# Optimization experiments

Hardware: AMD Instinct MI355X
Metric: run time of the kernel (lower is better)

The kernel has to match this reference:

```python
import jax, jax.numpy as jnp
import numpy as np

T, U, I, B, K = 64, 142, 4500, 16384, 10


def setup_inputs() -> dict:
    key = jax.random.key(0)
    k1, k2, k3, k4, k5, k6 = jax.random.split(key, 6)
    q = jax.random.uniform(k1, (T, U, I), dtype=jnp.float32, minval=0.01, maxval=5.0)
    miss = jax.random.uniform(k2, (T, U, I)) < 0.3
    qos_tensor = jnp.where(miss, 0.0, q)
    # user_avg exactly as in __init__: sum over items / count of rated items (clamped >= 1)
    cnt = jnp.clip((qos_tensor > 0).sum(axis=2).astype(jnp.float32), 1.0, None)
    user_avg = qos_tensor.sum(axis=2) / cnt  # [T, U]
    # time-aggregated similarity: random symmetric matrix in [-1, 1]
    s = jax.random.uniform(k3, (U, U), dtype=jnp.float32, minval=-1.0, maxval=1.0)
    user_sim_agg = 0.5 * (s + s.T)
    user_id = jax.random.randint(k4, (B,), 0, U)
    item_id = jax.random.randint(k5, (B,), 0, I)
    time_id = jax.random.randint(k6, (B,), 0, T)
    return {
        "qos_tensor": qos_tensor,
        "user_avg": user_avg,
        "user_sim_agg": user_sim_agg,
        "user_id": user_id,
        "item_id": item_id,
        "time_id": time_id,
        "top_k": K,
    }


def reference(qos_tensor, user_avg, user_sim_agg, user_id, item_id, time_id, top_k):
    num_users = qos_tensor.shape[1]
    avg_u = user_avg[time_id, user_id]                      # [B]
    sim_u = user_sim_agg[user_id]                           # [B, U]
    # ratings of every user for (time_id, item_id): column gather, [B, U]
    u_idx = jnp.arange(num_users)[None, :]
    item_col = qos_tensor[time_id[:, None], u_idx, item_id[:, None]]
    item_rated = item_col > 0                               # [B, U]
    sim_m = jnp.where(item_rated, sim_u, 0.0)
    top_sim, top_user = jax.lax.top_k(sim_m, top_k)         # [B, K]
    top_sim = top_sim / (top_sim.sum(axis=1, keepdims=True) + 1e-8)
    top_sim = jnp.nan_to_num(top_sim)
    # neighbor ratings and neighbor averages
    r_vs = qos_tensor[time_id[:, None], top_user, item_id[:, None]]  # [B, K]
    avg_v = user_avg[time_id[:, None], top_user]                     # [B, K]
    pred = avg_u + (top_sim * (r_vs - avg_v)).sum(axis=1)            # [B]
    return pred
```

## Files before the change

kernel.cpp:

```cpp
#include <hip/hip_runtime.h>
#include <math.h>

#define T_DIM 64
#define U_DIM 142
#define I_DIM 4500
#define B_DIM 16384
#define K_TOP 10

__global__ __launch_bounds__(256) void ucf_kernel(
    const float* __restrict__ qos,
    const float* __restrict__ user_avg,
    const float* __restrict__ user_sim,
    const int*   __restrict__ user_id,
    const int*   __restrict__ item_id,
    const int*   __restrict__ time_id,
    float*       __restrict__ out)
{
    const int lane = threadIdx.x & 63;
    const int wid  = threadIdx.x >> 6;
    const int b    = blockIdx.x * 4 + wid;
    if (b >= B_DIM) return;

    const int u = user_id[b];
    const int i = item_id[b];
    const int t = time_id[b];

    const float* qcol = qos + ((size_t)t * U_DIM) * (size_t)I_DIM + i;
    const float* srow = user_sim + (size_t)u * U_DIM;
    const float* arow = user_avg + (size_t)t * U_DIM;

    float val[3];
    float con[3];
#pragma unroll
    for (int j = 0; j < 3; ++j) {
        const int v = lane + j * 64;
        float sv = -INFINITY;
        float cv = 0.0f;
        if (v < U_DIM) {
            const float rv = qcol[(size_t)v * I_DIM];
            const float av = arow[v];
            const float s  = srow[v];
            sv = (rv > 0.0f) ? s : 0.0f;
            cv = sv * (rv - av);
        }
        val[j] = sv;
        con[j] = cv;
    }

    float ssum = 0.0f;
    float wsum = 0.0f;
#pragma unroll
    for (int k = 0; k < K_TOP; ++k) {
        float mv = val[0]; float mc = con[0]; int mk = lane;
        if (val[1] > mv) { mv = val[1]; mc = con[1]; mk = lane + 64; }
        if (val[2] > mv) { mv = val[2]; mc = con[2]; mk = lane + 128; }
#pragma unroll
        for (int off = 32; off > 0; off >>= 1) {
            const float ov = __shfl_xor(mv, off, 64);
            const float oc = __shfl_xor(mc, off, 64);
            const int   ok = __shfl_xor(mk, off, 64);
            if (ov > mv || (ov == mv && ok < mk)) { mv = ov; mc = oc; mk = ok; }
        }
        ssum += mv;
        wsum += mc;
        if ((mk & 63) == lane) {
            const int slot = mk >> 6;
            if (slot == 0)      val[0] = -INFINITY;
            else if (slot == 1) val[1] = -INFINITY;
            else                val[2] = -INFINITY;
        }
    }

    if (lane == 0) {
        const float avg_u = arow[u];
        out[b] = avg_u + wsum / (ssum + 1e-8f);
    }
}

extern "C" void kernel_launch(void* const* d_in, const int* in_sizes, int n_in,
                              void* d_out, int out_size, void* d_ws, size_t ws_size,
                              hipStream_t stream) {
    const float* qos  = (const float*)d_in[0];
    const float* uavg = (const float*)d_in[1];
    const float* usim = (const float*)d_in[2];
    const int*   uid  = (const int*)d_in[3];
    const int*   iid  = (const int*)d_in[4];
    const int*   tid  = (const int*)d_in[5];
    float* out = (float*)d_out;

    dim3 block(256);
    dim3 grid(B_DIM / 4);
    ucf_kernel<<<grid, block, 0, stream>>>(qos, uavg, usim, uid, iid, tid, out);
}
```

Measured before the change: 248.6 us.

## Stream QoS tensor coalesced into compact per-query rating rows before top-k

Measured after the change: 368.4 us. 1.48x slower.

```diff
diff --git a/kernel.cpp b/kernel.cpp
--- a/kernel.cpp
+++ b/kernel.cpp
@@ -6,49 +6,87 @@
 #define I_DIM 4500
 #define B_DIM 16384
 #define K_TOP 10
+#define U_PAD 144
 
-__global__ __launch_bounds__(256) void ucf_kernel(
-    const float* __restrict__ qos,
+__global__ __launch_bounds__(256) void k_clear(int* __restrict__ slotmap) {
+    const int idx = blockIdx.x * 256 + threadIdx.x;
+    slotmap[idx] = -1;
+}
+
+__global__ __launch_bounds__(256) void k_assign(const int* __restrict__ iid,
+                                                const int* __restrict__ tid,
+                                                int* __restrict__ slotmap) {
+    const int b  = blockIdx.x * 256 + threadIdx.x;
+    const int ti = tid[b] * I_DIM + iid[b];
+    atomicCAS(&slotmap[ti], -1, b);
+}
+
+__global__ __launch_bounds__(256) void k_extract(const float* __restrict__ qos,
+                                                 const int* __restrict__ slotmap,
+                                                 float* __restrict__ compact) {
+    const int lane = threadIdx.x & 63;
+    const int w    = threadIdx.x >> 6;
+    const int t    = blockIdx.y;
+    const int u0   = blockIdx.x * 16;
+    const int4* smap4 = (const int4*)(slotmap + (size_t)t * I_DIM);
+#pragma unroll
+    for (int r = 0; r < 4; ++r) {
+        const int u = u0 + w + r * 4;
+        if (u >= U_DIM) break;
+        const float4* row4 = (const float4*)(qos + ((size_t)t * U_DIM + u) * I_DIM);
+        for (int it = 0; it < 18; ++it) {
+            const int idx4 = it * 64 + lane;
+            if (idx4 < 1125) {
+                const float4 qv = row4[idx4];
+                const int4   ov = smap4[idx4];
+                if (ov.x >= 0) compact[(size_t)ov.x * U_PAD + u] = qv.x;
+                if (ov.y >= 0) compact[(size_t)ov.y * U_PAD + u] = qv.y;
+                if (ov.z >= 0) compact[(size_t)ov.z * U_PAD + u] = qv.z;
+                if (ov.w >= 0) compact[(size_t)ov.w * U_PAD + u] = qv.w;
+            }
+        }
+    }
+}
+
+__global__ __launch_bounds__(256) void k_final(
+    const float* __restrict__ compact,
     const float* __restrict__ user_avg,
     const float* __restrict__ user_sim,
-    const int*   __restrict__ user_id,
-    const int*   __restrict__ item_id,
-    const int*   __restrict__ time_id,
+    const int*   __restrict__ uid,
+    const int*   __restrict__ iid,
+    const int*   __restrict__ tid,
+    const int*   __restrict__ slotmap,
     float*       __restrict__ out)
 {
     const int lane = threadIdx.x & 63;
     const int wid  = threadIdx.x >> 6;
     const int b    = blockIdx.x * 4 + wid;
-    if (b >= B_DIM) return;
 
-    const int u = user_id[b];
-    const int i = item_id[b];
-    const int t = time_id[b];
+    const int u = uid[b];
+    const int i = iid[b];
+    const int t = tid[b];
+    const int o = slotmap[t * I_DIM + i];
 
-    const float* qcol = qos + ((size_t)t * U_DIM) * (size_t)I_DIM + i;
+    const float* crow = compact + (size_t)o * U_PAD;
     const float* srow = user_sim + (size_t)u * U_DIM;
     const float* arow = user_avg + (size_t)t * U_DIM;
 
-    float val[3];
-    float con[3];
+    float val[3], con[3];
 #pragma unroll
     for (int j = 0; j < 3; ++j) {
         const int v = lane + j * 64;
-        float sv = -INFINITY;
-        float cv = 0.0f;
+        float sv = -INFINITY, cv = 0.0f;
         if (v < U_DIM) {
-            const float rv = qcol[(size_t)v * I_DIM];
+            const float rv = crow[v];
             const float av = arow[v];
             const float s  = srow[v];
             sv = (rv > 0.0f) ? s : 0.0f;
             cv = sv * (rv - av);
         }
-        val[j] = sv;
-        con[j] = cv;
+        val[j] = sv; con[j] = cv;
     }
 
-    float ssum = 0.0f;
-    float wsum = 0.0f;
+    float ssum = 0.0f, wsum = 0.0f;
 #pragma unroll
     for (int k = 0; k < K_TOP; ++k) {
         float mv = val[0]; float mc = con[0]; int mk = lane;
@@ -61,8 +99,7 @@
             const int   ok = __shfl_xor(mk, off, 64);
             if (ov > mv || (ov == mv && ok < mk)) { mv = ov; mc = oc; mk = ok; }
         }
-        ssum += mv;
-        wsum += mc;
+        ssum += mv; wsum += mc;
         if ((mk & 63) == lane) {
             const int slot = mk >> 6;
             if (slot == 0)      val[0] = -INFINITY;
@@ -71,10 +108,56 @@
         }
     }
 
-    if (lane == 0) {
-        const float avg_u = arow[u];
-        out[b] = avg_u + wsum / (ssum + 1e-8f);
+    if (lane == 0) out[b] = arow[u] + wsum / (ssum + 1e-8f);
+}
+
+__global__ __launch_bounds__(256) void ucf_fallback(
+    const float* __restrict__ qos, const float* __restrict__ user_avg,
+    const float* __restrict__ user_sim, const int* __restrict__ uid,
+    const int* __restrict__ iid, const int* __restrict__ tid,
+    float* __restrict__ out)
+{
+    const int lane = threadIdx.x & 63;
+    const int wid  = threadIdx.x >> 6;
+    const int b    = blockIdx.x * 4 + wid;
+    const int u = uid[b], i = iid[b], t = tid[b];
+    const float* qcol = qos + ((size_t)t * U_DIM) * (size_t)I_DIM + i;
+    const float* srow = user_sim + (size_t)u * U_DIM;
+    const float* arow = user_avg + (size_t)t * U_DIM;
+    float val[3], con[3];
+#pragma unroll
+    for (int j = 0; j < 3; ++j) {
+        const int v = lane + j * 64;
+        float sv = -INFINITY, cv = 0.0f;
+        if (v < U_DIM) {
+            const float rv = qcol[(size_t)v * I_DIM];
+            sv = (rv > 0.0f) ? srow[v] : 0.0f;
+            cv = sv * (rv - arow[v]);
+        }
+        val[j] = sv; con[j] = cv;
     }
+    float ssum = 0.0f, wsum = 0.0f;
+#pragma unroll
+    for (int k = 0; k < K_TOP; ++k) {
+        float mv = val[0]; float mc = con[0]; int mk = lane;
+        if (val[1] > mv) { mv = val[1]; mc = con[1]; mk = lane + 64; }
+        if (val[2] > mv) { mv = val[2]; mc = con[2]; mk = lane + 128; }
+#pragma unroll
+        for (int off = 32; off > 0; off >>= 1) {
+            const float ov = __shfl_xor(mv, off, 64);
+            const float oc = __shfl_xor(mc, off, 64);
+            const int   ok = __shfl_xor(mk, off, 64);
+            if (ov > mv || (ov == mv && ok < mk)) { mv = ov; mc = oc; mk = ok; }
+        }
+        ssum += mv; wsum += mc;
+        if ((mk & 63) == lane) {
+            const int slot = mk >> 6;
+            if (slot == 0)      val[0] = -INFINITY;
+            else if (slot == 1) val[1] = -INFINITY;
+            else                val[2] = -INFINITY;
+        }
+    }
+    if (lane == 0) out[b] = arow[u] + wsum / (ssum + 1e-8f);
 }
 
 extern "C" void kernel_launch(void* const* d_in, const int* in_sizes, int n_in,
@@ -88,7 +171,21 @@
     const int*   tid  = (const int*)d_in[5];
     float* out = (float*)d_out;
 
-    dim3 block(256);
-    dim3 grid(B_DIM / 4);
-    ucf_kernel<<<grid, block, 0, stream>>>(qos, uavg, usim, uid, iid, tid, out);
+    const size_t smap_bytes = (size_t)T_DIM * I_DIM * sizeof(int);
+    const size_t off_compact = (smap_bytes + 255) & ~(size_t)255;
+    const size_t need = off_compact + (size_t)B_DIM * U_PAD * sizeof(float);
+
+    if (ws_size >= need) {
+        int*   slotmap = (int*)d_ws;
+        float* compact = (float*)((char*)d_ws + off_compact);
+
+        k_clear  <<<(T_DIM * I_DIM) / 256, 256, 0, stream>>>(slotmap);
+        k_assign <<<B_DIM / 256,           256, 0, stream>>>(iid, tid, slotmap);
+        dim3 eg((U_DIM + 15) / 16, T_DIM);
+        k_extract<<<eg,                    256, 0, stream>>>(qos, slotmap, compact);
+        k_final  <<<B_DIM / 4,             256, 0, stream>>>(compact, uavg, usim,
+                                                             uid, iid, tid, slotmap, out);
+    } else {
+        ucf_fallback<<<B_DIM / 4, 256, 0, stream>>>(qos, uavg, usim, uid, iid, tid, out);
+    }
 }
```
